# Kernel tuning notes

Hardware: AMD Instinct MI355X
Metric: run time of the kernel (lower is better)

The kernel has to match this reference:

```python
import jax, jax.numpy as jnp
import numpy as np

B, S, D = 4, 1024, 1024
H, DK, DV = 16, 64, 64


def setup_inputs() -> dict:
    key = jax.random.key(0)
    ks = jax.random.split(key, 8)
    sc = 0.02
    return {
        "queries": jax.random.normal(ks[0], (B, S, D), jnp.float32),
        "keys": jax.random.normal(ks[1], (B, S, D), jnp.float32),
        "values": jax.random.normal(ks[2], (B, S, D), jnp.float32),
        "attn_bias": jax.random.normal(ks[3], (B, 1, S, S), jnp.float32),
        "Wq": jax.random.normal(ks[4], (H * DK, D), jnp.float32) * sc,
        "Wk": jax.random.normal(ks[5], (H * DK, D), jnp.float32) * sc,
        "Wv": jax.random.normal(ks[6], (H * DV, D), jnp.float32) * sc,
        "Wp": jax.random.normal(ks[7], (D, H * DV), jnp.float32) * sc,
    }


def reference(queries, keys, values, attn_bias, Wq, Wk, Wv, Wp):
    # Linear (no bias): x @ W.T, then split heads -> [B, H, S, d]
    q = (queries @ Wq.T).reshape(B, S, H, DK).transpose(0, 2, 1, 3)
    k = (keys @ Wk.T).reshape(B, S, H, DK).transpose(0, 2, 1, 3)
    v = (values @ Wv.T).reshape(B, S, H, DV).transpose(0, 2, 1, 3)
    # NOTE: original scales by d_model**-0.5, not d_key**-0.5
    scores = jnp.einsum("bhqd,bhkd->bhqk", q, k) * (D ** -0.5)
    scores = scores + attn_bias  # bias broadcasts over heads
    weights = jax.nn.softmax(scores, axis=-1)
    out = jnp.einsum("bhqk,bhkd->bhqd", weights, v)  # [B,H,S,DV]
    out = out.transpose(0, 2, 1, 3).reshape(B, S, H * DV)
    return out @ Wp.T
```

## Files before the change

### kernel.cpp

```cpp
#include <hip/hip_runtime.h>
#include <hip/hip_bf16.h>

typedef unsigned short u16;
typedef unsigned int u32;
typedef __attribute__((ext_vector_type(8))) short bf16x8;
typedef __attribute__((ext_vector_type(8))) u16 u16x8;
typedef __attribute__((ext_vector_type(4))) u16 u16x4;
typedef __attribute__((ext_vector_type(4))) u32 u32x4;
typedef __attribute__((ext_vector_type(4))) float f32x4;
typedef __attribute__((ext_vector_type(4))) _Float16 f16x4;
typedef __attribute__((ext_vector_type(8))) _Float16 f16x8;
typedef __attribute__((ext_vector_type(16))) float f32x16;

typedef const __attribute__((address_space(1))) void* gas1_t;
typedef __attribute__((address_space(3))) void* las3_t;

#define MFMA16(a,b,c) __builtin_amdgcn_mfma_f32_16x16x32_bf16((a),(b),(c),0,0,0)
#define MFMA32(a,b,c) __builtin_amdgcn_mfma_f32_32x32x16_bf16((a),(b),(c),0,0,0)

static constexpr int BB = 4, SS = 1024, DD = 1024, HH = 16;

static __device__ __forceinline__ u16 f2b(float x) {
  union { __hip_bfloat16 h; u16 u; } cv;
  cv.h = __float2bfloat16(x);
  return cv.u;
}
static __device__ __forceinline__ u32 pk2(float a, float b) {
  return (u32)f2b(a) | ((u32)f2b(b) << 16);
}

__global__ __launch_bounds__(256) void cvt_all(
    const float* __restrict__ q, const float* __restrict__ k, const float* __restrict__ v,
    const float* __restrict__ wq_, const float* __restrict__ wk_, const float* __restrict__ wv_,
    const float* __restrict__ wp_, const float* __restrict__ bias,
    u16* __restrict__ qb, u16* __restrict__ kb, u16* __restrict__ vb,
    u16* __restrict__ wqb, u16* __restrict__ wkb, u16* __restrict__ wvb, u16* __restrict__ wpb,
    _Float16* __restrict__ bias16) {
  int bid = blockIdx.x;
  if (bid >= 16384) {
    int i = ((bid - 16384) * 256 + threadIdx.x) * 4;
    int row = i >> 10;
    int kk_ = i & 1023;
    int b_ = row >> 10, qq = row & 1023;
    int qt = qq >> 7, wq = (qq >> 5) & 3, ln = qq & 31;
    int kt = kk_ >> 6, kk = kk_ & 63;
    int kbf = kk >> 5, rem = kk & 31, rq = rem >> 3, inner = rem & 7;
    int hi = inner >> 2;
    int g = kbf * 2 + (rq >> 1);
    int ctid = wq * 64 + hi * 32 + ln;
    size_t tile = ((size_t)(b_ * 8 + qt) * 16 + kt) << 13;
    float4 val = *(const float4*)(bias + i);
    f16x4 r = { (_Float16)val.x, (_Float16)val.y, (_Float16)val.z, (_Float16)val.w };
    *(f16x4*)(bias16 + tile + g * 2048 + ctid * 8 + (rq & 1) * 4) = r;
    return;
  }
  const float* s; u16* d; int off;
  if      (bid < 4096)  { s = q;   d = qb;  off = bid; }
  else if (bid < 8192)  { s = k;   d = kb;  off = bid - 4096; }
  else if (bid < 12288) { s = v;   d = vb;  off = bid - 8192; }
  else if (bid < 13312) { s = wq_; d = wqb; off = bid - 12288; }
  else if (bid < 14336) { s = wk_; d = wkb; off = bid - 13312; }
  else if (bid < 15360) { s = wv_; d = wvb; off = bid - 14336; }
  else                  { s = wp_; d = wpb; off = bid - 15360; }
  int i = (off * 256 + threadIdx.x) * 4;
  float4 val = *(const float4*)(s + i);
  u16x4 r = { f2b(val.x), f2b(val.y), f2b(val.z), f2b(val.w) };
  *(u16x4*)(d + i) = r;
}

template<typename OT, bool VTRANS>
__global__ __launch_bounds__(256) void gemm_bt(
    const u16* __restrict__ Abase, const u16* __restrict__ Wbase, OT* __restrict__ Cbase,
    u16* __restrict__ Tout, int N, int K, size_t sA, size_t sW, size_t sC) {
  const u16* A = Abase + (size_t)blockIdx.z * sA;
  const u16* W = Wbase + (size_t)blockIdx.z * sW;
  OT* C = Cbase + (size_t)blockIdx.z * sC;

  __shared__ __align__(16) u16 As[128 * 64];
  __shared__ __align__(16) u16 Bs[128 * 64];

  const int tid = threadIdx.x;
  const int lane = tid & 63;
  const int wid = tid >> 6;
  const int g = lane >> 4;
  const int li = lane & 15;

  const int hw = blockIdx.x + (blockIdx.y << 3);
  const int L = ((hw & 7) << 5) + (hw >> 3);
  const int brow = (L >> 3) * 128;
  const int bcol = (L & 7) * 128;

  const int wr = (wid >> 1) * 64;
  const int wc = (wid & 1) * 64;

  const int srow = wid * 8 + (lane >> 3);
  const int schunk = (lane & 7) ^ (lane >> 3);
  const u16* ga0 = A + (size_t)(brow + srow) * K + schunk * 8;
  const u16* gw0 = W + (size_t)(bcol + srow) * K + schunk * 8;

  f32x4 acc[4][4] = {};

  for (int k0 = 0; k0 < K; k0 += 64) {
#pragma unroll
    for (int i = 0; i < 4; ++i) {
      __builtin_amdgcn_global_load_lds((gas1_t)(const void*)(ga0 + (size_t)(i * 32) * K + k0),
                                       (las3_t)(void*)(As + (i * 32 + wid * 8) * 64), 16, 0, 0);
      __builtin_amdgcn_global_load_lds((gas1_t)(const void*)(gw0 + (size_t)(i * 32) * K + k0),
                                       (las3_t)(void*)(Bs + (i * 32 + wid * 8) * 64), 16, 0, 0);
    }
    __syncthreads();

#pragma unroll
    for (int kk = 0; kk < 2; ++kk) {
      bf16x8 a[4], b[4];
#pragma unroll
      for (int m = 0; m < 4; ++m) {
        int row = wr + m * 16 + li;
        a[m] = *(const bf16x8*)&As[row * 64 + (((kk * 4 + g) ^ (li & 7)) << 3)];
      }
#pragma unroll
      for (int n = 0; n < 4; ++n) {
        int row = wc + n * 16 + li;
        b[n] = *(const bf16x8*)&Bs[row * 64 + (((kk * 4 + g) ^ (li & 7)) << 3)];
      }
#pragma unroll
      for (int m = 0; m < 4; ++m)
#pragma unroll
        for (int n = 0; n < 4; ++n)
          acc[m][n] = MFMA16(a[m], b[n], acc[m][n]);
    }
    __syncthreads();
  }

  if (VTRANS && blockIdx.z == 2) {
#pragma unroll
    for (int m = 0; m < 4; ++m) {
#pragma unroll
      for (int n = 0; n < 4; ++n) {
        int c = bcol + wc + n * 16 + li;
        int h_ = c >> 6, dv = c & 63;
        int r0 = brow + wr + m * 16 + g * 4;
        int b_ = r0 >> 10, s0 = r0 & 1023;
        u16x4 val = { f2b(acc[m][n][0]), f2b(acc[m][n][1]),
                      f2b(acc[m][n][2]), f2b(acc[m][n][3]) };
        *(u16x4*)&Tout[(size_t)((b_ * HH + h_) * 64 + dv) * SS + s0] = val;
      }
    }
  } else {
#pragma unroll
    for (int m = 0; m < 4; ++m)
#pragma unroll
      for (int n = 0; n < 4; ++n)
#pragma unroll
        for (int j = 0; j < 4; ++j) {
          int r = brow + wr + m * 16 + g * 4 + j;
          int c = bcol + wc + n * 16 + li;
          if constexpr (sizeof(OT) == 2) C[(size_t)r * N + c] = (OT)f2b(acc[m][n][j]);
          else                           C[(size_t)r * N + c] = acc[m][n][j];
        }
  }
}

__global__ __launch_bounds__(256) void attn_kernel(
    const u16* __restrict__ Q, const u16* __restrict__ K, const u16* __restrict__ Vt,
    const _Float16* __restrict__ bias16, u16* __restrict__ O) {
  __shared__ __align__(16) u16 kbuf[2][64 * 64];
  __shared__ __align__(16) u16 vbuf[2][64 * 64];

  const int tid = threadIdx.x;
  const int lane = tid & 63;
  const int wq = tid >> 6;
  const int hi = lane >> 5;
  const int ln = lane & 31;
  const u32 swz = (u32)(ln & 7) << 4;

  const int flat = blockIdx.x + (blockIdx.y << 3) + (blockIdx.z << 7);
  const int L = ((flat & 7) << 6) | (flat >> 3);
  const int qt = L & 7, h = (L >> 3) & 15, b = L >> 7;
  const int q0 = qt * 128;
  const int qrow = q0 + wq * 32 + ln;

  bf16x8 qf[4];
  {
    const u16* qp = Q + (size_t)(b * SS + qrow) * DD + h * 64 + hi * 8;
#pragma unroll
    for (int d = 0; d < 4; ++d) qf[d] = *(const bf16x8*)(qp + d * 16);
  }

  const int srow = (lane >> 3);
  const int spc = ((lane & 7) ^ srow) * 8;
  const u16* kgl = K + (size_t)(b * SS + wq * 16 + srow) * DD + h * 64 + spc;
  const u16* vgl = Vt + (size_t)((b * HH + h) * 64 + wq * 16 + srow) * SS + spc;

  const _Float16* btile = bias16 + (((size_t)(b * 8 + qt) * 16) << 13) + tid * 8;

  {
    char* kd = (char*)kbuf[0] + wq * 2048;
    char* vd = (char*)vbuf[0] + wq * 2048;
#pragma unroll
    for (int j = 0; j < 2; ++j) {
      __builtin_amdgcn_global_load_lds((gas1_t)(const void*)(kgl + (size_t)(j * 8) * DD),
                                       (las3_t)(void*)(kd + j * 1024), 16, 0, 0);
      __builtin_amdgcn_global_load_lds((gas1_t)(const void*)(vgl + (size_t)(j * 8) * SS),
                                       (las3_t)(void*)(vd + j * 1024), 16, 0, 0);
    }
  }
  f16x8 bbr[4], bbn[4];
#pragma unroll
  for (int g = 0; g < 4; ++g)
    bbr[g] = *(const f16x8*)(btile + g * 2048);
  __syncthreads();

  f32x16 o0 = {}, o1 = {};
  float m = -1e30f, lsum = 0.f;
  int cur = 0;

  for (int kt = 0; kt < 16; ++kt) {
    if (kt < 15) {
      char* kd = (char*)kbuf[cur ^ 1] + wq * 2048;
      char* vd = (char*)vbuf[cur ^ 1] + wq * 2048;
      const size_t k1 = (size_t)(kt + 1) * 64;
#pragma unroll
      for (int j = 0; j < 2; ++j) {
        __builtin_amdgcn_global_load_lds((gas1_t)(const void*)(kgl + (k1 + j * 8) * DD),
                                         (las3_t)(void*)(kd + j * 1024), 16, 0, 0);
        __builtin_amdgcn_global_load_lds((gas1_t)(const void*)(vgl + (size_t)(j * 8) * SS + k1),
                                         (las3_t)(void*)(vd + j * 1024), 16, 0, 0);
      }
      const _Float16* bt = btile + ((size_t)(kt + 1) << 13);
#pragma unroll
      for (int g = 0; g < 4; ++g)
        bbn[g] = *(const f16x8*)(bt + g * 2048);
    }

    const char* kb_base = (const char*)kbuf[cur];
    f32x16 s[2];
#pragma unroll
    for (int kb = 0; kb < 2; ++kb) {
      f32x16 acc = {};
#pragma unroll
      for (int d = 0; d < 4; ++d) {
        bf16x8 kf = *(const bf16x8*)(kb_base + (kb * 32 + ln) * 128 + (((u32)(d * 32 + hi * 16)) ^ swz));
        acc = MFMA32(kf, qf[d], acc);
      }
      s[kb] = acc;
    }

#pragma unroll
    for (int g = 0; g < 4; ++g) {
      const int kb = g >> 1, rq0 = (g & 1) * 2;
#pragma unroll
      for (int e = 0; e < 8; ++e)
        s[kb][(rq0 + (e >> 2)) * 4 + (e & 3)] =
            fmaf(s[kb][(rq0 + (e >> 2)) * 4 + (e & 3)], 0.03125f, (float)bbr[g][e]);
    }

    float mt = -1e30f;
#pragma unroll
    for (int r = 0; r < 16; ++r) { mt = fmaxf(mt, s[0][r]); mt = fmaxf(mt, s[1][r]); }
    mt = fmaxf(mt, __shfl_xor(mt, 32));

    bool resc = false;
    float fsc = 1.f;
    if (kt == 0) {
      m = mt;
    } else if (__any(mt > m + 8.f)) {
      float mn = fmaxf(m, mt);
      fsc = __expf(m - mn);
      m = mn;
      resc = true;
    }

    float rs = 0.f;
    u32 wv[2][8];
#pragma unroll
    for (int kb = 0; kb < 2; ++kb)
#pragma unroll
      for (int t = 0; t < 8; ++t) {
        float p0 = __expf(s[kb][2 * t] - m);
        float p1 = __expf(s[kb][2 * t + 1] - m);
        rs += p0 + p1;
        wv[kb][t] = pk2(p0, p1);
      }
    rs += __shfl_xor(rs, 32);
    lsum = lsum * fsc + rs;

    if (resc) {
#pragma unroll
      for (int j = 0; j < 16; ++j) {
        float fv = __shfl(fsc, (j & 3) + 8 * (j >> 2) + 4 * hi);
        o0[j] *= fv; o1[j] *= fv;
      }
    }

    const char* vb_base = (const char*)vbuf[cur];
#pragma unroll
    for (int ks = 0; ks < 4; ++ks) {
      const int kb = ks >> 1, i0 = (ks & 1) * 4;
      u32 sA = hi ? wv[kb][i0 + 0] : wv[kb][i0 + 2];
      u32 sB = hi ? wv[kb][i0 + 1] : wv[kb][i0 + 3];
      u32 rA = (u32)__shfl_xor((int)sA, 32);
      u32 rB = (u32)__shfl_xor((int)sB, 32);
      u32 e0 = hi ? rA : wv[kb][i0 + 0];
      u32 e1 = hi ? rB : wv[kb][i0 + 1];
      u32 e2 = hi ? wv[kb][i0 + 2] : rA;
      u32 e3 = hi ? wv[kb][i0 + 3] : rB;
      union { u32x4 u; bf16x8 v; } pc;
      pc.u = (u32x4){e0, e1, e2, e3};
      bf16x8 pa = pc.v;
#pragma unroll
      for (int nv = 0; nv < 2; ++nv) {
        bf16x8 vf = *(const bf16x8*)(vb_base + (nv * 32 + ln) * 128 + (((u32)(ks * 32 + hi * 16)) ^ swz));
        if (nv == 0) o0 = MFMA32(pa, vf, o0);
        else         o1 = MFMA32(pa, vf, o1);
      }
    }

    if (kt < 15) {
      __syncthreads();
      cur ^= 1;
#pragma unroll
      for (int g = 0; g < 4; ++g) bbr[g] = bbn[g];
    }
  }

  float inv = 1.0f / lsum;
#pragma unroll
  for (int j = 0; j < 16; ++j) {
    float iv = __shfl(inv, (j & 3) + 8 * (j >> 2) + 4 * hi);
    int q = q0 + wq * 32 + (j & 3) + 8 * (j >> 2) + 4 * hi;
    u16* op = O + (size_t)(b * SS + q) * DD + h * 64 + ln;
    op[0]  = f2b(o0[j] * iv);
    op[32] = f2b(o1[j] * iv);
  }
}

extern "C" void kernel_launch(void* const* d_in, const int* in_sizes, int n_in,
                              void* d_out, int out_size, void* d_ws, size_t ws_size,
                              hipStream_t stream) {
  const float* queries = (const float*)d_in[0];
  const float* keys    = (const float*)d_in[1];
  const float* values  = (const float*)d_in[2];
  const float* bias    = (const float*)d_in[3];
  const float* Wq      = (const float*)d_in[4];
  const float* Wk      = (const float*)d_in[5];
  const float* Wv      = (const float*)d_in[6];
  const float* Wp      = (const float*)d_in[7];
  float* out = (float*)d_out;

  char* ws = (char*)d_ws;
  const size_t MB = 1024 * 1024;
  u16* qb  = (u16*)(ws + 0 * MB);
  u16* kb  = (u16*)(ws + 8 * MB);
  u16* vb  = (u16*)(ws + 16 * MB);
  u16* wqb = (u16*)(ws + 24 * MB);
  u16* wkb = (u16*)(ws + 26 * MB);
  u16* wvb = (u16*)(ws + 28 * MB);
  u16* wpb = (u16*)(ws + 30 * MB);
  u16* Qb  = (u16*)(ws + 32 * MB);
  u16* Kb  = (u16*)(ws + 40 * MB);
  _Float16* bias16 = (_Float16*)(ws + 48 * MB);
  u16* Vtb = (u16*)(ws + 56 * MB);
  u16* Ob  = (u16*)(ws + 0 * MB);

  const int nAct = BB * SS * DD;
  const int nW = DD * DD;

  cvt_all<<<dim3(20480), dim3(256), 0, stream>>>(
      queries, keys, values, Wq, Wk, Wv, Wp, bias,
      qb, kb, vb, wqb, wkb, wvb, wpb, bias16);

  gemm_bt<u16, true><<<dim3(8, 32, 3), dim3(256), 0, stream>>>(
      qb, wqb, Qb, Vtb, DD, DD, (size_t)nAct, (size_t)nW, (size_t)nAct);

  attn_kernel<<<dim3(8, 16, 4), dim3(256), 0, stream>>>(Qb, Kb, Vtb, bias16, Ob);

  gemm_bt<float, false><<<dim3(8, 32, 1), dim3(256), 0, stream>>>(
      Ob, wpb, out, nullptr, DD, DD, 0, 0, 0);
}
```

Before: 122.0 us.

## Add dedicated 512-thread output projection GEMM and vectorize bias conversion writes

The output projection now runs in a new gemm_proj kernel with 512 threads (8 waves, each computing a 32x64 tile), in place of the generic 256-thread gemm_bt. The aim is more waves per block and lower register pressure per wave, which should improve latency hiding. Separately, the bias conversion is re-indexed so each thread writes one contiguous 8-half f16 chunk from two float4 loads, halving the number of bias blocks launched. The new GEMM has a single LDS buffer with no double buffering, so it may stall between k-steps.

```diff
diff --git a/kernel.cpp b/kernel.cpp
--- a/kernel.cpp
+++ b/kernel.cpp
@@ -38,20 +38,21 @@
     _Float16* __restrict__ bias16) {
   int bid = blockIdx.x;
   if (bid >= 16384) {
-    int i = ((bid - 16384) * 256 + threadIdx.x) * 4;
-    int row = i >> 10;
-    int kk_ = i & 1023;
-    int b_ = row >> 10, qq = row & 1023;
-    int qt = qq >> 7, wq = (qq >> 5) & 3, ln = qq & 31;
-    int kt = kk_ >> 6, kk = kk_ & 63;
-    int kbf = kk >> 5, rem = kk & 31, rq = rem >> 3, inner = rem & 7;
-    int hi = inner >> 2;
-    int g = kbf * 2 + (rq >> 1);
-    int ctid = wq * 64 + hi * 32 + ln;
-    size_t tile = ((size_t)(b_ * 8 + qt) * 16 + kt) << 13;
-    float4 val = *(const float4*)(bias + i);
-    f16x4 r = { (_Float16)val.x, (_Float16)val.y, (_Float16)val.z, (_Float16)val.w };
-    *(f16x4*)(bias16 + tile + g * 2048 + ctid * 8 + (rq & 1) * 4) = r;
+    int G = (bid - 16384) * 256 + threadIdx.x;
+    int gi = G & 1023;
+    int ctid = gi & 255, g = gi >> 8;
+    int T = G >> 10;
+    int kt = T & 15, qt = (T >> 4) & 7, b_ = T >> 7;
+    int wq = ctid >> 6, hi = (ctid >> 5) & 1, ln = ctid & 31;
+    int qrow = qt * 128 + wq * 32 + ln;
+    int kbf = g >> 1, j = g & 1;
+    int k0 = kt * 64 + kbf * 32 + j * 16 + hi * 4;
+    const float* src = bias + (((size_t)(b_ * 1024 + qrow)) << 10) + k0;
+    float4 lo = *(const float4*)(src);
+    float4 up = *(const float4*)(src + 8);
+    f16x8 r = { (_Float16)lo.x, (_Float16)lo.y, (_Float16)lo.z, (_Float16)lo.w,
+                (_Float16)up.x, (_Float16)up.y, (_Float16)up.z, (_Float16)up.w };
+    *(f16x8*)(bias16 + (((size_t)T) << 13) + g * 2048 + ctid * 8) = r;
     return;
   }
   const float* s; u16* d; int off;
@@ -159,6 +160,77 @@
           else                           C[(size_t)r * N + c] = acc[m][n][j];
         }
   }
+}
+
+__global__ __launch_bounds__(512) void gemm_proj(
+    const u16* __restrict__ A, const u16* __restrict__ W, float* __restrict__ C,
+    int N, int K) {
+  __shared__ __align__(16) u16 As[128 * 64];
+  __shared__ __align__(16) u16 Bs[128 * 64];
+
+  const int tid = threadIdx.x;
+  const int lane = tid & 63;
+  const int wid = tid >> 6;
+  const int g = lane >> 4;
+  const int li = lane & 15;
+
+  const int hw = blockIdx.x + (blockIdx.y << 3);
+  const int L = ((hw & 7) << 5) + (hw >> 3);
+  const int brow = (L >> 3) * 128;
+  const int bcol = (L & 7) * 128;
+
+  const int wr = (wid >> 1) * 32;
+  const int wc = (wid & 1) * 64;
+
+  const int srow = tid >> 3;
+  const int schunk = (tid & 7) ^ (srow & 7);
+  const u16* ga0 = A + (size_t)(brow + srow) * K + schunk * 8;
+  const u16* gw0 = W + (size_t)(bcol + srow) * K + schunk * 8;
+
+  f32x4 acc[2][4] = {};
+
+  for (int k0 = 0; k0 < K; k0 += 64) {
+#pragma unroll
+    for (int i = 0; i < 2; ++i) {
+      __builtin_amdgcn_global_load_lds((gas1_t)(const void*)(ga0 + (size_t)(i * 64) * K + k0),
+                                       (las3_t)(void*)(As + (i * 64 + (wid << 3)) * 64), 16, 0, 0);
+      __builtin_amdgcn_global_load_lds((gas1_t)(const void*)(gw0 + (size_t)(i * 64) * K + k0),
+                                       (las3_t)(void*)(Bs + (i * 64 + (wid << 3)) * 64), 16, 0, 0);
+    }
+    __syncthreads();
+
+#pragma unroll
+    for (int kk = 0; kk < 2; ++kk) {
+      bf16x8 a[2], b[4];
+#pragma unroll
+      for (int m = 0; m < 2; ++m) {
+        int row = wr + m * 16 + li;
+        a[m] = *(const bf16x8*)&As[row * 64 + (((kk * 4 + g) ^ (li & 7)) << 3)];
+      }
+#pragma unroll
+      for (int n = 0; n < 4; ++n) {
+        int row = wc + n * 16 + li;
+        b[n] = *(const bf16x8*)&Bs[row * 64 + (((kk * 4 + g) ^ (li & 7)) << 3)];
+      }
+#pragma unroll
+      for (int m = 0; m < 2; ++m)
+#pragma unroll
+        for (int n = 0; n < 4; ++n)
+          acc[m][n] = MFMA16(a[m], b[n], acc[m][n]);
+    }
+    __syncthreads();
+  }
+
+#pragma unroll
+  for (int m = 0; m < 2; ++m)
+#pragma unroll
+    for (int n = 0; n < 4; ++n)
+#pragma unroll
+      for (int j = 0; j < 4; ++j) {
+        int r = brow + wr + m * 16 + g * 4 + j;
+        int c = bcol + wc + n * 16 + li;
+        C[(size_t)r * N + c] = acc[m][n][j];
+      }
 }
 
 __global__ __launch_bounds__(256) void attn_kernel(
@@ -366,7 +438,7 @@
   const int nAct = BB * SS * DD;
   const int nW = DD * DD;
 
-  cvt_all<<<dim3(20480), dim3(256), 0, stream>>>(
+  cvt_all<<<dim3(18432), dim3(256), 0, stream>>>(
       queries, keys, values, Wq, Wk, Wv, Wp, bias,
       qb, kb, vb, wqb, wkb, wvb, wpb, bias16);
 
@@ -375,6 +447,5 @@
 
   attn_kernel<<<dim3(8, 16, 4), dim3(256), 0, stream>>>(Qb, Kb, Vtb, bias16, Ob);
 
-  gemm_bt<float, false><<<dim3(8, 32, 1), dim3(256), 0, stream>>>(
-      Ob, wpb, out, nullptr, DD, DD, 0, 0, 0);
-}
+  gemm_proj<<<dim3(8, 32), dim3(512), 0, stream>>>(Ob, wpb, out, DD, DD);
+}
```

After: 117.4 us. 1.04x faster.

## Use 512-thread GEMM blocks and write bias conversion with 16-byte stores

Applied to the files above, without the earlier changes.

The projection GEMMs now launch 512 threads (8 waves) per 128x128 tile, each wave computing a 32x64 sub-tile instead of 64x64, so there are more waves to hide latency and fewer accumulator registers per thread. The bias fp32->fp16 conversion kernel is reorganised so each thread produces one contiguous 8-element fp16 chunk of the tiled layout, writing 16-byte stores instead of scattered 8-byte ones, with half the blocks. The GEMM change trades register reuse per wave for occupancy and adds more LDS fragment reads per MFMA.

```diff
diff --git a/kernel.cpp b/kernel.cpp
--- a/kernel.cpp
+++ b/kernel.cpp
@@ -38,20 +38,21 @@
     _Float16* __restrict__ bias16) {
   int bid = blockIdx.x;
   if (bid >= 16384) {
-    int i = ((bid - 16384) * 256 + threadIdx.x) * 4;
-    int row = i >> 10;
-    int kk_ = i & 1023;
-    int b_ = row >> 10, qq = row & 1023;
-    int qt = qq >> 7, wq = (qq >> 5) & 3, ln = qq & 31;
-    int kt = kk_ >> 6, kk = kk_ & 63;
-    int kbf = kk >> 5, rem = kk & 31, rq = rem >> 3, inner = rem & 7;
-    int hi = inner >> 2;
-    int g = kbf * 2 + (rq >> 1);
-    int ctid = wq * 64 + hi * 32 + ln;
-    size_t tile = ((size_t)(b_ * 8 + qt) * 16 + kt) << 13;
-    float4 val = *(const float4*)(bias + i);
-    f16x4 r = { (_Float16)val.x, (_Float16)val.y, (_Float16)val.z, (_Float16)val.w };
-    *(f16x4*)(bias16 + tile + g * 2048 + ctid * 8 + (rq & 1) * 4) = r;
+    int G = (bid - 16384) * 256 + threadIdx.x;
+    int gi = G & 1023;
+    int ctid = gi & 255, g = gi >> 8;
+    int T = G >> 10;
+    int kt = T & 15, qt = (T >> 4) & 7, b_ = T >> 7;
+    int wq = ctid >> 6, hi = (ctid >> 5) & 1, ln = ctid & 31;
+    int qrow = qt * 128 + wq * 32 + ln;
+    int kbf = g >> 1, j = g & 1;
+    int k0 = kt * 64 + kbf * 32 + j * 16 + hi * 4;
+    const float* src = bias + (((size_t)(b_ * 1024 + qrow)) << 10) + k0;
+    float4 lo = *(const float4*)(src);
+    float4 up = *(const float4*)(src + 8);
+    f16x8 r = { (_Float16)lo.x, (_Float16)lo.y, (_Float16)lo.z, (_Float16)lo.w,
+                (_Float16)up.x, (_Float16)up.y, (_Float16)up.z, (_Float16)up.w };
+    *(f16x8*)(bias16 + (((size_t)T) << 13) + g * 2048 + ctid * 8) = r;
     return;
   }
   const float* s; u16* d; int off;
@@ -69,7 +70,7 @@
 }
 
 template<typename OT, bool VTRANS>
-__global__ __launch_bounds__(256) void gemm_bt(
+__global__ __launch_bounds__(512) void gemm_bt512(
     const u16* __restrict__ Abase, const u16* __restrict__ Wbase, OT* __restrict__ Cbase,
     u16* __restrict__ Tout, int N, int K, size_t sA, size_t sW, size_t sC) {
   const u16* A = Abase + (size_t)blockIdx.z * sA;
@@ -90,31 +91,31 @@
   const int brow = (L >> 3) * 128;
   const int bcol = (L & 7) * 128;
 
-  const int wr = (wid >> 1) * 64;
+  const int wr = (wid >> 1) * 32;
   const int wc = (wid & 1) * 64;
 
-  const int srow = wid * 8 + (lane >> 3);
-  const int schunk = (lane & 7) ^ (lane >> 3);
+  const int srow = tid >> 3;
+  const int schunk = (tid & 7) ^ (srow & 7);
   const u16* ga0 = A + (size_t)(brow + srow) * K + schunk * 8;
   const u16* gw0 = W + (size_t)(bcol + srow) * K + schunk * 8;
 
-  f32x4 acc[4][4] = {};
+  f32x4 acc[2][4] = {};
 
   for (int k0 = 0; k0 < K; k0 += 64) {
 #pragma unroll
-    for (int i = 0; i < 4; ++i) {
-      __builtin_amdgcn_global_load_lds((gas1_t)(const void*)(ga0 + (size_t)(i * 32) * K + k0),
-                                       (las3_t)(void*)(As + (i * 32 + wid * 8) * 64), 16, 0, 0);
-      __builtin_amdgcn_global_load_lds((gas1_t)(const void*)(gw0 + (size_t)(i * 32) * K + k0),
-                                       (las3_t)(void*)(Bs + (i * 32 + wid * 8) * 64), 16, 0, 0);
+    for (int i = 0; i < 2; ++i) {
+      __builtin_amdgcn_global_load_lds((gas1_t)(const void*)(ga0 + (size_t)(i * 64) * K + k0),
+                                       (las3_t)(void*)(As + (i * 64 + (wid << 3)) * 64), 16, 0, 0);
+      __builtin_amdgcn_global_load_lds((gas1_t)(const void*)(gw0 + (size_t)(i * 64) * K + k0),
+                                       (las3_t)(void*)(Bs + (i * 64 + (wid << 3)) * 64), 16, 0, 0);
     }
     __syncthreads();
 
 #pragma unroll
     for (int kk = 0; kk < 2; ++kk) {
-      bf16x8 a[4], b[4];
-#pragma unroll
-      for (int m = 0; m < 4; ++m) {
+      bf16x8 a[2], b[4];
+#pragma unroll
+      for (int m = 0; m < 2; ++m) {
         int row = wr + m * 16 + li;
         a[m] = *(const bf16x8*)&As[row * 64 + (((kk * 4 + g) ^ (li & 7)) << 3)];
       }
@@ -124,7 +125,7 @@
         b[n] = *(const bf16x8*)&Bs[row * 64 + (((kk * 4 + g) ^ (li & 7)) << 3)];
       }
 #pragma unroll
-      for (int m = 0; m < 4; ++m)
+      for (int m = 0; m < 2; ++m)
 #pragma unroll
         for (int n = 0; n < 4; ++n)
           acc[m][n] = MFMA16(a[m], b[n], acc[m][n]);
@@ -134,7 +135,7 @@
 
   if (VTRANS && blockIdx.z == 2) {
 #pragma unroll
-    for (int m = 0; m < 4; ++m) {
+    for (int m = 0; m < 2; ++m) {
 #pragma unroll
       for (int n = 0; n < 4; ++n) {
         int c = bcol + wc + n * 16 + li;
@@ -148,7 +149,7 @@
     }
   } else {
 #pragma unroll
-    for (int m = 0; m < 4; ++m)
+    for (int m = 0; m < 2; ++m)
 #pragma unroll
       for (int n = 0; n < 4; ++n)
 #pragma unroll
@@ -366,15 +367,15 @@
   const int nAct = BB * SS * DD;
   const int nW = DD * DD;
 
-  cvt_all<<<dim3(20480), dim3(256), 0, stream>>>(
+  cvt_all<<<dim3(18432), dim3(256), 0, stream>>>(
       queries, keys, values, Wq, Wk, Wv, Wp, bias,
       qb, kb, vb, wqb, wkb, wvb, wpb, bias16);
 
-  gemm_bt<u16, true><<<dim3(8, 32, 3), dim3(256), 0, stream>>>(
+  gemm_bt512<u16, true><<<dim3(8, 32, 3), dim3(512), 0, stream>>>(
       qb, wqb, Qb, Vtb, DD, DD, (size_t)nAct, (size_t)nW, (size_t)nAct);
 
   attn_kernel<<<dim3(8, 16, 4), dim3(256), 0, stream>>>(Qb, Kb, Vtb, bias16, Ob);
 
-  gemm_bt<float, false><<<dim3(8, 32, 1), dim3(256), 0, stream>>>(
+  gemm_bt512<float, false><<<dim3(8, 32, 1), dim3(512), 0, stream>>>(
       Ob, wpb, out, nullptr, DD, DD, 0, 0, 0);
 }
```

Result: faster. 114.4 us (-6.3%).
